# Optimization experiments

Hardware: AMD Instinct MI355X
Metric: run time of the kernel (lower is better)

Reference implementation:

```python
import jax, jax.numpy as jnp
import numpy as np

B, C, L = 256, 256, 512
EPS = 1e-5

def setup_inputs() -> dict:
    key = jax.random.key(0)
    k1, k2, k3, k4 = jax.random.split(key, 4)
    x = jax.random.normal(k1, (B, C, L), dtype=jnp.float32)
    idx = jax.random.randint(k2, (B, L), 0, L + 1, dtype=jnp.int32)  # L == pad slot
    # Conv1d(2C, C, 1): weight [C, 2C], bias [C]
    W = jax.random.normal(k3, (C, 2 * C), dtype=jnp.float32) * (1.0 / np.sqrt(2 * C))
    b = jax.random.normal(k4, (C,), dtype=jnp.float32) * 0.01
    return {"x": x, "idx": idx, "W": W, "b": b}

def reference(x, idx, W, b):
    # collect_neighbours: pad length dim with one zero column, gather per (b, l)
    x_pad = jnp.pad(x, ((0, 0), (0, 0), (0, 1)))            # [B, C, L+1]
    nbr = jnp.take_along_axis(x_pad, idx[:, None, :].astype(jnp.int32), axis=2)  # [B, C, L]
    cat = jnp.concatenate([x, nbr], axis=1)                 # [B, 2C, L]
    # 1x1 Conv1d == channel matmul
    y = jnp.einsum('oc,bcl->bol', W, cat) + b[None, :, None]  # [B, C, L]
    # InstanceNorm1d (affine=False): normalize over L per (b, c), biased var
    mu = jnp.mean(y, axis=2, keepdims=True)
    var = jnp.mean(jnp.square(y - mu), axis=2, keepdims=True)
    y = (y - mu) * jax.lax.rsqrt(var + EPS)
    return jax.nn.relu(y)
```

## Files before the change

### kernel.cpp

```cpp
#include <hip/hip_runtime.h>
#include <hip/hip_bf16.h>
#include <stdint.h>

typedef __bf16 bf16x8 __attribute__((ext_vector_type(8)));
typedef float  f32x4  __attribute__((ext_vector_type(4)));

__device__ __forceinline__ uint32_t cvt2(float a, float b) {
    __hip_bfloat162 h = __float22bfloat162_rn(make_float2(a, b));
    uint32_t u; __builtin_memcpy(&u, &h, 4); return u;
}
__device__ __forceinline__ float bflo(uint32_t u) { uint32_t t = u << 16;         float f; __builtin_memcpy(&f, &t, 4); return f; }
__device__ __forceinline__ float bfhi(uint32_t u) { uint32_t t = u & 0xffff0000u; float f; __builtin_memcpy(&f, &t, 4); return f; }
__device__ __forceinline__ int swz(int u) { return u ^ ((u >> 3) & 7); }

__device__ __forceinline__ void gload_lds16(const void* g, void* l) {
    __builtin_amdgcn_global_load_lds(
        (const __attribute__((address_space(1))) uint32_t*)g,
        (__attribute__((address_space(3))) uint32_t*)l,
        16, 0, 0);
}

__global__ __launch_bounds__(256, 4)
void pack_transpose(const float* __restrict__ x, const float* __restrict__ W,
                    unsigned short* __restrict__ xT, unsigned short* __restrict__ wT)
{
    const int tid = threadIdx.x;
    const int id  = blockIdx.x;
    if (id < 2048) {
        const int b  = ((id >> 6) << 3) + (id & 7);
        const int kc = (id >> 3) & 7;
        const int s2 = tid >> 6, l4 = tid & 63;
        const float* src0 = x + ((size_t)b << 17) + ((size_t)((kc << 5) + (s2 << 3)) << 9);
        unsigned short* dst0 = xT + (((size_t)(b << 5) + (kc << 2) + s2) << 12);
        f32x4 xr[16];
        #pragma unroll
        for (int lh = 0; lh < 2; ++lh) {
            const int l0 = (lh << 8) + (l4 << 2);
            #pragma unroll
            for (int j = 0; j < 8; ++j)
                xr[(lh << 3) + j] = __builtin_nontemporal_load((const f32x4*)(src0 + (j << 9) + l0));
        }
        #pragma unroll
        for (int lh = 0; lh < 2; ++lh) {
            const int l0 = (lh << 8) + (l4 << 2);
            #pragma unroll
            for (int lv = 0; lv < 4; ++lv) {
                uint4 p;
                p.x = cvt2(xr[(lh << 3) + 0][lv], xr[(lh << 3) + 1][lv]);
                p.y = cvt2(xr[(lh << 3) + 2][lv], xr[(lh << 3) + 3][lv]);
                p.z = cvt2(xr[(lh << 3) + 4][lv], xr[(lh << 3) + 5][lv]);
                p.w = cvt2(xr[(lh << 3) + 6][lv], xr[(lh << 3) + 7][lv]);
                *(uint4*)(dst0 + ((l0 + lv) << 3)) = p;
            }
        }
    } else {
        const int og = id - 2048;
        const int r = tid & 63, sg = tid >> 6;
        const float* wrow = W + ((size_t)((og << 5) + (r & 31)) << 9) + ((r >> 5) << 8);
        #pragma unroll
        for (int ss = 0; ss < 8; ++ss) {
            const int s = (sg << 3) + ss;
            float4 f0 = *(const float4*)(wrow + (s << 3));
            float4 f1 = *(const float4*)(wrow + (s << 3) + 4);
            uint4 p;
            p.x = cvt2(f0.x, f0.y); p.y = cvt2(f0.z, f0.w);
            p.z = cvt2(f1.x, f1.y); p.w = cvt2(f1.z, f1.w);
            *(uint4*)(wT + (((((og << 5) + s) << 6) + r) << 3)) = p;
        }
    }
}

__global__ __launch_bounds__(256, 2)
void edge_gemm(const unsigned short* __restrict__ xT,
               const unsigned short* __restrict__ wT,
               const int* __restrict__ idx,
               float* __restrict__ out)
{
    __shared__ __align__(16) unsigned char smem[76032];
    unsigned short* y2 = (unsigned short*)(smem + 36864);
    float* red         = (float*)(smem + 75776);

    const int tid  = threadIdx.x;
    const int wv   = tid >> 6;
    const int lane = tid & 63;
    const int m    = lane & 15;
    const int q    = lane >> 4;

    const int id  = blockIdx.x;
    const int rem = id & 63;
    const int b   = ((id >> 6) << 3) + (rem & 7);
    const int og  = rem >> 3;
    const int o0  = og << 5;

    const char* xb = (const char*)xT + ((size_t)b << 18);
    const char* wb = (const char*)wT + (og << 15);

    const int offS = (wv << 10) + (lane << 4);

    int iv[8];
    #pragma unroll
    for (int nt = 0; nt < 8; ++nt)
        iv[nt] = idx[((size_t)b << 9) + (wv << 7) + (nt << 4) + m];

    f32x4 acc[4][8];
    #pragma unroll
    for (int mt = 0; mt < 4; ++mt)
        #pragma unroll
        for (int nt = 0; nt < 8; ++nt)
            acc[mt][nt] = (f32x4){0.f, 0.f, 0.f, 0.f};

    auto stage = [&](int c, int bsel) {
        char* Bl = (char*)smem + bsel * 36864;
        const char* Bg = xb + ((size_t)c << 15);
        #pragma unroll
        for (int i = 0; i < 8; ++i)
            gload_lds16(Bg + (i << 12) + offS, Bl + (i << 12) + offS);
        gload_lds16(wb + (c << 12) + offS, Bl + 32768 + offS);
    };

    stage(0, 1);
    stage(1, 0);

    #pragma unroll
    for (int kc = 0; kc < 8; ++kc) {
        const int bsel = (kc + 1) & 1;
        if (kc < 7) asm volatile("s_waitcnt vmcnt(9)" ::: "memory");
        else        asm volatile("s_waitcnt vmcnt(0)" ::: "memory");
        __builtin_amdgcn_s_barrier();
        __builtin_amdgcn_sched_barrier(0);

        const unsigned short* B0 = (const unsigned short*)((const char*)smem + bsel * 36864);
        const unsigned short* A0 = B0 + 16384;
        bf16x8 av[4], bv[8];
        #pragma unroll
        for (int mt = 0; mt < 4; ++mt)
            av[mt] = *(const bf16x8*)(A0 + (q << 9) + (((mt << 4) + m) << 3));
        #pragma unroll
        for (int nt = 0; nt < 8; ++nt)
            bv[nt] = *(const bf16x8*)(B0 + (q << 12) + (((wv << 7) + (nt << 4) + m) << 3));
        #pragma unroll
        for (int mt = 0; mt < 4; ++mt)
            #pragma unroll
            for (int nt = 0; nt < 8; ++nt)
                acc[mt][nt] = __builtin_amdgcn_mfma_f32_16x16x32_bf16(av[mt], bv[nt], acc[mt][nt], 0, 0, 0);

        __builtin_amdgcn_sched_barrier(0);
        if (kc < 7) {
            asm volatile("s_waitcnt lgkmcnt(0)" ::: "memory");
            __builtin_amdgcn_s_barrier();
            if (kc < 6) stage(kc + 2, bsel);
        }
    }

    #pragma unroll
    for (int mt = 2; mt < 4; ++mt)
        #pragma unroll
        for (int nt = 0; nt < 8; ++nt) {
            int col  = (wv << 7) + (nt << 4) + m;
            int row0 = ((mt - 2) << 4) + (q << 2);
            uint2 p;
            p.x = cvt2(acc[mt][nt][0], acc[mt][nt][1]);
            p.y = cvt2(acc[mt][nt][2], acc[mt][nt][3]);
            *(uint2*)(y2 + col * 38 + row0) = p;
        }
    __syncthreads();

    float vvl[2][8][4];
    float s_[2][4], q_[2][4];
    #pragma unroll
    for (int mt = 0; mt < 2; ++mt)
        #pragma unroll
        for (int r4 = 0; r4 < 4; ++r4) { s_[mt][r4] = 0.f; q_[mt][r4] = 0.f; }

    #pragma unroll
    for (int nt = 0; nt < 8; ++nt) {
        int  c   = iv[nt];
        bool inb = (c < 512);
        int  cc  = inb ? c : 0;
        #pragma unroll
        for (int mt = 0; mt < 2; ++mt) {
            uint2 g = *(const uint2*)(y2 + cc * 38 + (mt << 4) + (q << 2));
            float gv[4];
            gv[0] = inb ? bflo(g.x) : 0.f;
            gv[1] = inb ? bfhi(g.x) : 0.f;
            gv[2] = inb ? bflo(g.y) : 0.f;
            gv[3] = inb ? bfhi(g.y) : 0.f;
            #pragma unroll
            for (int r4 = 0; r4 < 4; ++r4) {
                float val = acc[mt][nt][r4] + gv[r4];
                vvl[mt][nt][r4] = val;
                s_[mt][r4] += val;
                q_[mt][r4] += val * val;
            }
        }
    }

    #pragma unroll
    for (int mt = 0; mt < 2; ++mt)
        #pragma unroll
        for (int r4 = 0; r4 < 4; ++r4) {
            float s = s_[mt][r4], ss = q_[mt][r4];
            #pragma unroll
            for (int off = 1; off < 16; off <<= 1) {
                s  += __shfl_xor(s,  off, 64);
                ss += __shfl_xor(ss, off, 64);
            }
            if (m == 0) {
                int r = (mt << 4) + (q << 2) + r4;
                red[(r << 3) + (wv << 1)]     = s;
                red[(r << 3) + (wv << 1) + 1] = ss;
            }
        }
    __syncthreads();

    #pragma unroll
    for (int mt = 0; mt < 2; ++mt)
        #pragma unroll
        for (int r4 = 0; r4 < 4; ++r4) {
            int r = (mt << 4) + (q << 2) + r4;
            float S = red[(r << 3)]     + red[(r << 3) + 2] + red[(r << 3) + 4] + red[(r << 3) + 6];
            float Q = red[(r << 3) + 1] + red[(r << 3) + 3] + red[(r << 3) + 5] + red[(r << 3) + 7];
            float mu  = S * (1.0f / 512.0f);
            float var = Q * (1.0f / 512.0f) - mu * mu;
            float rs  = rsqrtf(var + 1e-5f);
            float* op = out + (((size_t)(b << 8) + o0 + r) << 9) + (wv << 7) + m;
            #pragma unroll
            for (int nt = 0; nt < 8; ++nt) {
                float t = (vvl[mt][nt][r4] - mu) * rs;
                __builtin_nontemporal_store(fmaxf(t, 0.0f), op + (nt << 4));
            }
        }
}

__global__ __launch_bounds__(256, 2)
void edgeconv_fused(const float* __restrict__ x,
                    const int*   __restrict__ idx,
                    const float* __restrict__ W,
                    float*       __restrict__ out)
{
    __shared__ __align__(16) unsigned char smem[65536];
    unsigned short* wlds = (unsigned short*)smem;
    unsigned short* xTl  = (unsigned short*)(smem + 32768);
    unsigned short* y2   = (unsigned short*)smem;
    float*          red  = (float*)(smem + 38912);

    const int tid  = threadIdx.x;
    const int wv   = tid >> 6;
    const int lane = tid & 63;
    const int m    = lane & 15;
    const int q    = lane >> 4;

    const int id  = blockIdx.x;
    const int rem = id & 63;
    const int b   = ((id >> 6) << 3) + (rem & 7);
    const int o0  = (rem >> 3) << 5;

    const float* xb = x + ((size_t)b << 17);

    #pragma unroll
    for (int i = 0; i < 16; ++i) {
        int r = (i << 2) + wv;
        const float4 f = *(const float4*)(W + ((size_t)(o0 + (r & 31)) << 9)
                                            + ((r >> 5) << 8) + (lane << 2));
        uint2 p; p.x = cvt2(f.x, f.y); p.y = cvt2(f.z, f.w);
        int sl = lane >> 1;
        *(uint2*)(wlds + (sl << 9) + ((swz(r) ^ (sl & 7)) << 3) + ((lane & 1) << 2)) = p;
    }

    f32x4 acc[4][8];
    #pragma unroll
    for (int mt = 0; mt < 4; ++mt)
        #pragma unroll
        for (int nt = 0; nt < 8; ++nt)
            acc[mt][nt] = (f32x4){0.f, 0.f, 0.f, 0.f};

    float4 xr0[8], xr1[8];
    auto loadg = [&](int kc, int g, float4* xr) {
        int gid = (g << 8) + tid;
        int s2  = gid >> 7;
        int l4  = gid & 127;
        const float* base = xb + ((size_t)((kc << 5) + (s2 << 3)) << 9) + (l4 << 2);
        #pragma unroll
        for (int j = 0; j < 8; ++j) xr[j] = *(const float4*)(base + (j << 9));
    };
    auto storeg = [&](int g, const float4* xr) {
        int gid = (g << 8) + tid;
        int s2  = gid >> 7;
        int l4  = gid & 127;
        #pragma unroll
        for (int lv = 0; lv < 4; ++lv) {
            int l = (l4 << 2) + lv;
            uint4 p;
            p.x = cvt2((&xr[0].x)[lv], (&xr[1].x)[lv]);
            p.y = cvt2((&xr[2].x)[lv], (&xr[3].x)[lv]);
            p.z = cvt2((&xr[4].x)[lv], (&xr[5].x)[lv]);
            p.w = cvt2((&xr[6].x)[lv], (&xr[7].x)[lv]);
            *(uint4*)(xTl + (s2 << 12) + (swz(l) << 3)) = p;
        }
    };

    loadg(0, 0, xr0);
    loadg(0, 1, xr1);
    storeg(0, xr0);
    storeg(1, xr1);
    __syncthreads();

    for (int kc = 0; kc < 8; ++kc) {
        if (kc < 7) loadg(kc + 1, 0, xr0);

        bf16x8 av[4], bv[8];
        #pragma unroll
        for (int mt = 0; mt < 4; ++mt) {
            int sl = (kc << 2) + q;
            av[mt] = *(const bf16x8*)(wlds + (sl << 9) + ((swz((mt << 4) + m) ^ (sl & 7)) << 3));
        }
        #pragma unroll
        for (int nt = 0; nt < 8; ++nt)
            bv[nt] = *(const bf16x8*)(xTl + (q << 12) + (swz((wv << 7) + (nt << 4) + m) << 3));

        #pragma unroll
        for (int mt = 0; mt < 4; ++mt)
            #pragma unroll
            for (int nt = 0; nt < 8; ++nt)
                acc[mt][nt] = __builtin_amdgcn_mfma_f32_16x16x32_bf16(av[mt], bv[nt], acc[mt][nt], 0, 0, 0);

        if (kc < 7) loadg(kc + 1, 1, xr1);
        __syncthreads();
        if (kc < 7) {
            storeg(0, xr0);
            storeg(1, xr1);
            __syncthreads();
        }
    }

    int iv[8];
    #pragma unroll
    for (int nt = 0; nt < 8; ++nt)
        iv[nt] = idx[((size_t)b << 9) + (wv << 7) + (nt << 4) + m];

    #pragma unroll
    for (int mt = 2; mt < 4; ++mt)
        #pragma unroll
        for (int nt = 0; nt < 8; ++nt) {
            int col  = (wv << 7) + (nt << 4) + m;
            int row0 = ((mt - 2) << 4) + (q << 2);
            uint2 p;
            p.x = cvt2(acc[mt][nt][0], acc[mt][nt][1]);
            p.y = cvt2(acc[mt][nt][2], acc[mt][nt][3]);
            *(uint2*)(y2 + col * 36 + row0) = p;
        }
    __syncthreads();

    float vvl[2][8][4];
    float s_[2][4], q_[2][4];
    #pragma unroll
    for (int mt = 0; mt < 2; ++mt)
        #pragma unroll
        for (int r4 = 0; r4 < 4; ++r4) { s_[mt][r4] = 0.f; q_[mt][r4] = 0.f; }

    #pragma unroll
    for (int nt = 0; nt < 8; ++nt) {
        int  c   = iv[nt];
        bool inb = (c < 512);
        int  cc  = inb ? c : 0;
        #pragma unroll
        for (int mt = 0; mt < 2; ++mt) {
            uint2 g = *(const uint2*)(y2 + cc * 36 + (mt << 4) + (q << 2));
            float gv[4];
            gv[0] = inb ? bflo(g.x) : 0.f;
            gv[1] = inb ? bfhi(g.x) : 0.f;
            gv[2] = inb ? bflo(g.y) : 0.f;
            gv[3] = inb ? bfhi(g.y) : 0.f;
            #pragma unroll
            for (int r4 = 0; r4 < 4; ++r4) {
                float val = acc[mt][nt][r4] + gv[r4];
                vvl[mt][nt][r4] = val;
                s_[mt][r4] += val;
                q_[mt][r4] += val * val;
            }
        }
    }

    #pragma unroll
    for (int mt = 0; mt < 2; ++mt)
        #pragma unroll
        for (int r4 = 0; r4 < 4; ++r4) {
            float s = s_[mt][r4], ss = q_[mt][r4];
            #pragma unroll
            for (int off = 1; off < 16; off <<= 1) {
                s  += __shfl_xor(s,  off, 64);
                ss += __shfl_xor(ss, off, 64);
            }
            if (m == 0) {
                int r = (mt << 4) + (q << 2) + r4;
                red[(r << 3) + (wv << 1)]     = s;
                red[(r << 3) + (wv << 1) + 1] = ss;
            }
        }
    __syncthreads();

    #pragma unroll
    for (int mt = 0; mt < 2; ++mt)
        #pragma unroll
        for (int r4 = 0; r4 < 4; ++r4) {
            int r = (mt << 4) + (q << 2) + r4;
            float S = red[(r << 3)]     + red[(r << 3) + 2] + red[(r << 3) + 4] + red[(r << 3) + 6];
            float Q = red[(r << 3) + 1] + red[(r << 3) + 3] + red[(r << 3) + 5] + red[(r << 3) + 7];
            float mu  = S * (1.0f / 512.0f);
            float var = Q * (1.0f / 512.0f) - mu * mu;
            float rs  = rsqrtf(var + 1e-5f);
            float* op = out + (((size_t)(b << 8) + o0 + r) << 9) + (wv << 7) + m;
            #pragma unroll
            for (int nt = 0; nt < 8; ++nt) {
                float t = (vvl[mt][nt][r4] - mu) * rs;
                op[nt << 4] = fmaxf(t, 0.0f);
            }
        }
}

extern "C" void kernel_launch(void* const* d_in, const int* in_sizes, int n_in,
                              void* d_out, int out_size, void* d_ws, size_t ws_size,
                              hipStream_t stream) {
    const float* x   = (const float*)d_in[0];
    const int*   idx = (const int*)  d_in[1];
    const float* W   = (const float*)d_in[2];
    float* out = (float*)d_out;

    const size_t xT_bytes = (size_t)256 * 32 * 512 * 8 * 2;
    const size_t wT_bytes = (size_t)8 * 32 * 64 * 8 * 2;

    if (ws_size >= xT_bytes + wT_bytes) {
        unsigned short* xT = (unsigned short*)d_ws;
        unsigned short* wT = (unsigned short*)((char*)d_ws + xT_bytes);
        pack_transpose<<<dim3(2056), dim3(256), 0, stream>>>(x, W, xT, wT);
        edge_gemm<<<dim3(2048), dim3(256), 0, stream>>>(xT, wT, idx, out);
    } else {
        edgeconv_fused<<<dim3(2048), dim3(256), 0, stream>>>(x, idx, W, out);
    }
}
```

Baseline: 305.6 us.

## Share staged x tile across two output groups in 512-thread GEMM blocks

Edge GEMM blocks grow to 512 threads, with two 4-wave groups computing adjacent 32-row output slices against one shared staged x tile. This halves global reads of the activation tile and the number of blocks. The hand-tuned vmcnt/s_barrier pipeline is replaced by a plain double-buffered loop synchronised with __syncthreads, and the non-temporal output stores become ordinary stores. The launch bound of (512,4) may force a very tight register budget with 128 accumulator floats per thread, so spilling is a risk.

```diff
diff --git a/kernel.cpp b/kernel.cpp
--- a/kernel.cpp
+++ b/kernel.cpp
@@ -70,37 +70,39 @@
     }
 }
 
-__global__ __launch_bounds__(256, 2)
+__global__ __launch_bounds__(512, 4)
 void edge_gemm(const unsigned short* __restrict__ xT,
                const unsigned short* __restrict__ wT,
                const int* __restrict__ idx,
                float* __restrict__ out)
 {
-    __shared__ __align__(16) unsigned char smem[76032];
-    unsigned short* y2 = (unsigned short*)(smem + 36864);
-    float* red         = (float*)(smem + 75776);
+    __shared__ __align__(16) unsigned char smem[81920];
 
     const int tid  = threadIdx.x;
     const int wv   = tid >> 6;
     const int lane = tid & 63;
     const int m    = lane & 15;
     const int q    = lane >> 4;
+    const int g    = wv >> 2;
+    const int wsub = wv & 3;
 
     const int id  = blockIdx.x;
-    const int rem = id & 63;
-    const int b   = ((id >> 6) << 3) + (rem & 7);
-    const int og  = rem >> 3;
+    const int rem = id & 31;
+    const int b   = ((id >> 5) << 3) + (rem & 7);
+    const int ogp = rem >> 3;
+    const int og  = (ogp << 1) + g;
     const int o0  = og << 5;
 
     const char* xb = (const char*)xT + ((size_t)b << 18);
-    const char* wb = (const char*)wT + (og << 15);
-
-    const int offS = (wv << 10) + (lane << 4);
+    const char* wp = (const char*)wT + ((size_t)og << 15);
+
+    unsigned short* y2  = (unsigned short*)(smem + g * 40960);
+    float*          red = (float*)(smem + g * 40960 + 38912);
 
     int iv[8];
     #pragma unroll
     for (int nt = 0; nt < 8; ++nt)
-        iv[nt] = idx[((size_t)b << 9) + (wv << 7) + (nt << 4) + m];
+        iv[nt] = idx[((size_t)b << 9) + (wsub << 7) + (nt << 4) + m];
 
     f32x4 acc[4][8];
     #pragma unroll
@@ -109,54 +111,51 @@
         for (int nt = 0; nt < 8; ++nt)
             acc[mt][nt] = (f32x4){0.f, 0.f, 0.f, 0.f};
 
+    const int offB = tid << 4;
+    const int offA = (g << 12) + (wsub << 10) + (lane << 4);
+
     auto stage = [&](int c, int bsel) {
-        char* Bl = (char*)smem + bsel * 36864;
+        char* base = (char*)smem + bsel * 40960;
         const char* Bg = xb + ((size_t)c << 15);
         #pragma unroll
-        for (int i = 0; i < 8; ++i)
-            gload_lds16(Bg + (i << 12) + offS, Bl + (i << 12) + offS);
-        gload_lds16(wb + (c << 12) + offS, Bl + 32768 + offS);
+        for (int i = 0; i < 4; ++i)
+            gload_lds16(Bg + (i << 13) + offB, base + (i << 13) + offB);
+        gload_lds16(wp + (c << 12) + (wsub << 10) + (lane << 4), base + 32768 + offA);
     };
 
     stage(0, 1);
-    stage(1, 0);
+    __syncthreads();
 
     #pragma unroll
     for (int kc = 0; kc < 8; ++kc) {
         const int bsel = (kc + 1) & 1;
-        if (kc < 7) asm volatile("s_waitcnt vmcnt(9)" ::: "memory");
-        else        asm volatile("s_waitcnt vmcnt(0)" ::: "memory");
-        __builtin_amdgcn_s_barrier();
-        __builtin_amdgcn_sched_barrier(0);
-
-        const unsigned short* B0 = (const unsigned short*)((const char*)smem + bsel * 36864);
+        if (kc < 7) stage(kc + 1, bsel ^ 1);
+
+        const unsigned short* B0 = (const unsigned short*)((const char*)smem + bsel * 40960);
         const unsigned short* A0 = B0 + 16384;
         bf16x8 av[4], bv[8];
         #pragma unroll
         for (int mt = 0; mt < 4; ++mt)
-            av[mt] = *(const bf16x8*)(A0 + (q << 9) + (((mt << 4) + m) << 3));
+            av[mt] = *(const bf16x8*)(A0 + (g << 11) + (q << 9) + (((mt << 4) + m) << 3));
         #pragma unroll
         for (int nt = 0; nt < 8; ++nt)
-            bv[nt] = *(const bf16x8*)(B0 + (q << 12) + (((wv << 7) + (nt << 4) + m) << 3));
+            bv[nt] = *(const bf16x8*)(B0 + (q << 12) + (((wsub << 7) + (nt << 4) + m) << 3));
         #pragma unroll
         for (int mt = 0; mt < 4; ++mt)
             #pragma unroll
             for (int nt = 0; nt < 8; ++nt)
                 acc[mt][nt] = __builtin_amdgcn_mfma_f32_16x16x32_bf16(av[mt], bv[nt], acc[mt][nt], 0, 0, 0);
 
-        __builtin_amdgcn_sched_barrier(0);
-        if (kc < 7) {
-            asm volatile("s_waitcnt lgkmcnt(0)" ::: "memory");
-            __builtin_amdgcn_s_barrier();
-            if (kc < 6) stage(kc + 2, bsel);
-        }
-    }
+        if (kc < 7) __syncthreads();
+    }
+
+    __syncthreads();
 
     #pragma unroll
     for (int mt = 2; mt < 4; ++mt)
         #pragma unroll
         for (int nt = 0; nt < 8; ++nt) {
-            int col  = (wv << 7) + (nt << 4) + m;
+            int col  = (wsub << 7) + (nt << 4) + m;
             int row0 = ((mt - 2) << 4) + (q << 2);
             uint2 p;
             p.x = cvt2(acc[mt][nt][0], acc[mt][nt][1]);
@@ -179,12 +178,12 @@
         int  cc  = inb ? c : 0;
         #pragma unroll
         for (int mt = 0; mt < 2; ++mt) {
-            uint2 g = *(const uint2*)(y2 + cc * 38 + (mt << 4) + (q << 2));
+            uint2 gg = *(const uint2*)(y2 + cc * 38 + (mt << 4) + (q << 2));
             float gv[4];
-            gv[0] = inb ? bflo(g.x) : 0.f;
-            gv[1] = inb ? bfhi(g.x) : 0.f;
-            gv[2] = inb ? bflo(g.y) : 0.f;
-            gv[3] = inb ? bfhi(g.y) : 0.f;
+            gv[0] = inb ? bflo(gg.x) : 0.f;
+            gv[1] = inb ? bfhi(gg.x) : 0.f;
+            gv[2] = inb ? bflo(gg.y) : 0.f;
+            gv[3] = inb ? bfhi(gg.y) : 0.f;
             #pragma unroll
             for (int r4 = 0; r4 < 4; ++r4) {
                 float val = acc[mt][nt][r4] + gv[r4];
@@ -207,8 +206,8 @@
             }
             if (m == 0) {
                 int r = (mt << 4) + (q << 2) + r4;
-                red[(r << 3) + (wv << 1)]     = s;
-                red[(r << 3) + (wv << 1) + 1] = ss;
+                red[(r << 3) + (wsub << 1)]     = s;
+                red[(r << 3) + (wsub << 1) + 1] = ss;
             }
         }
     __syncthreads();
@@ -223,11 +222,11 @@
             float mu  = S * (1.0f / 512.0f);
             float var = Q * (1.0f / 512.0f) - mu * mu;
             float rs  = rsqrtf(var + 1e-5f);
-            float* op = out + (((size_t)(b << 8) + o0 + r) << 9) + (wv << 7) + m;
+            float* op = out + (((size_t)(b << 8) + o0 + r) << 9) + (wsub << 7) + m;
             #pragma unroll
             for (int nt = 0; nt < 8; ++nt) {
                 float t = (vvl[mt][nt][r4] - mu) * rs;
-                __builtin_nontemporal_store(fmaxf(t, 0.0f), op + (nt << 4));
+                op[nt << 4] = fmaxf(t, 0.0f);
             }
         }
 }
@@ -433,7 +432,7 @@
         unsigned short* xT = (unsigned short*)d_ws;
         unsigned short* wT = (unsigned short*)((char*)d_ws + xT_bytes);
         pack_transpose<<<dim3(2056), dim3(256), 0, stream>>>(x, W, xT, wT);
-        edge_gemm<<<dim3(2048), dim3(256), 0, stream>>>(xT, wT, idx, out);
+        edge_gemm<<<dim3(1024), dim3(512), 0, stream>>>(xT, wT, idx, out);
     } else {
         edgeconv_fused<<<dim3(2048), dim3(256), 0, stream>>>(x, idx, W, out);
     }
```

Result: slower. 497.3 us (+62.7%).

## Split edge_gemm across 8 waves with fewer accumulators and simpler double buffering

Applied to the files above, without the earlier changes.

The GEMM kernel now uses 512 threads per block. Each of the 8 waves owns 64 columns, so each wave holds half as many accumulators and the per-thread register pressure drops, which is meant to allow more resident waves. The hand-tuned vmcnt-based two-stage prefetch is replaced by a single-ahead prefetch with plain __syncthreads, and the stored vvl values are dropped: the gathered neighbour term is recomputed from LDS in a second pass. The y2 buffer now reuses the staging buffer's LDS space. The trade-offs are less overlap between memory loads and compute, extra LDS reads, and regular stores in place of nontemporal ones.

```diff
diff --git a/kernel.cpp b/kernel.cpp
--- a/kernel.cpp
+++ b/kernel.cpp
@@ -70,15 +70,15 @@
     }
 }
 
-__global__ __launch_bounds__(256, 2)
+__global__ __launch_bounds__(512, 4)
 void edge_gemm(const unsigned short* __restrict__ xT,
                const unsigned short* __restrict__ wT,
                const int* __restrict__ idx,
                float* __restrict__ out)
 {
-    __shared__ __align__(16) unsigned char smem[76032];
-    unsigned short* y2 = (unsigned short*)(smem + 36864);
-    float* red         = (float*)(smem + 75776);
+    __shared__ __align__(16) unsigned char smem[73728];
+    unsigned short* y2  = (unsigned short*)smem;
+    float*          red = (float*)(smem + 40960);
 
     const int tid  = threadIdx.x;
     const int wv   = tid >> 6;
@@ -95,68 +95,62 @@
     const char* xb = (const char*)xT + ((size_t)b << 18);
     const char* wb = (const char*)wT + (og << 15);
 
-    const int offS = (wv << 10) + (lane << 4);
-
-    int iv[8];
-    #pragma unroll
-    for (int nt = 0; nt < 8; ++nt)
-        iv[nt] = idx[((size_t)b << 9) + (wv << 7) + (nt << 4) + m];
-
-    f32x4 acc[4][8];
+    int iv[4];
+    #pragma unroll
+    for (int nt = 0; nt < 4; ++nt)
+        iv[nt] = idx[((size_t)b << 9) + (wv << 6) + (nt << 4) + m];
+
+    f32x4 acc[4][4];
     #pragma unroll
     for (int mt = 0; mt < 4; ++mt)
         #pragma unroll
-        for (int nt = 0; nt < 8; ++nt)
+        for (int nt = 0; nt < 4; ++nt)
             acc[mt][nt] = (f32x4){0.f, 0.f, 0.f, 0.f};
 
+    const int offB = tid << 4;
     auto stage = [&](int c, int bsel) {
-        char* Bl = (char*)smem + bsel * 36864;
+        char* base = (char*)smem + bsel * 36864;
         const char* Bg = xb + ((size_t)c << 15);
         #pragma unroll
-        for (int i = 0; i < 8; ++i)
-            gload_lds16(Bg + (i << 12) + offS, Bl + (i << 12) + offS);
-        gload_lds16(wb + (c << 12) + offS, Bl + 32768 + offS);
+        for (int i = 0; i < 4; ++i)
+            gload_lds16(Bg + (i << 13) + offB, base + (i << 13) + offB);
+        if (tid < 256)
+            gload_lds16(wb + (c << 12) + offB, base + 32768 + offB);
     };
 
-    stage(0, 1);
-    stage(1, 0);
+    stage(0, 0);
+    __syncthreads();
 
     #pragma unroll
     for (int kc = 0; kc < 8; ++kc) {
-        const int bsel = (kc + 1) & 1;
-        if (kc < 7) asm volatile("s_waitcnt vmcnt(9)" ::: "memory");
-        else        asm volatile("s_waitcnt vmcnt(0)" ::: "memory");
-        __builtin_amdgcn_s_barrier();
-        __builtin_amdgcn_sched_barrier(0);
+        const int bsel = kc & 1;
+        if (kc < 7) stage(kc + 1, bsel ^ 1);
 
         const unsigned short* B0 = (const unsigned short*)((const char*)smem + bsel * 36864);
         const unsigned short* A0 = B0 + 16384;
-        bf16x8 av[4], bv[8];
+        bf16x8 av[4], bv[4];
         #pragma unroll
         for (int mt = 0; mt < 4; ++mt)
             av[mt] = *(const bf16x8*)(A0 + (q << 9) + (((mt << 4) + m) << 3));
         #pragma unroll
-        for (int nt = 0; nt < 8; ++nt)
-            bv[nt] = *(const bf16x8*)(B0 + (q << 12) + (((wv << 7) + (nt << 4) + m) << 3));
+        for (int nt = 0; nt < 4; ++nt)
+            bv[nt] = *(const bf16x8*)(B0 + (q << 12) + (((wv << 6) + (nt << 4) + m) << 3));
         #pragma unroll
         for (int mt = 0; mt < 4; ++mt)
             #pragma unroll
-            for (int nt = 0; nt < 8; ++nt)
+            for (int nt = 0; nt < 4; ++nt)
                 acc[mt][nt] = __builtin_amdgcn_mfma_f32_16x16x32_bf16(av[mt], bv[nt], acc[mt][nt], 0, 0, 0);
 
-        __builtin_amdgcn_sched_barrier(0);
-        if (kc < 7) {
-            asm volatile("s_waitcnt lgkmcnt(0)" ::: "memory");
-            __builtin_amdgcn_s_barrier();
-            if (kc < 6) stage(kc + 2, bsel);
-        }
-    }
+        if (kc < 7) __syncthreads();
+    }
+
+    __syncthreads();
 
     #pragma unroll
     for (int mt = 2; mt < 4; ++mt)
         #pragma unroll
-        for (int nt = 0; nt < 8; ++nt) {
-            int col  = (wv << 7) + (nt << 4) + m;
+        for (int nt = 0; nt < 4; ++nt) {
+            int col  = (wv << 6) + (nt << 4) + m;
             int row0 = ((mt - 2) << 4) + (q << 2);
             uint2 p;
             p.x = cvt2(acc[mt][nt][0], acc[mt][nt][1]);
@@ -165,7 +159,6 @@
         }
     __syncthreads();
 
-    float vvl[2][8][4];
     float s_[2][4], q_[2][4];
     #pragma unroll
     for (int mt = 0; mt < 2; ++mt)
@@ -173,7 +166,7 @@
         for (int r4 = 0; r4 < 4; ++r4) { s_[mt][r4] = 0.f; q_[mt][r4] = 0.f; }
 
     #pragma unroll
-    for (int nt = 0; nt < 8; ++nt) {
+    for (int nt = 0; nt < 4; ++nt) {
         int  c   = iv[nt];
         bool inb = (c < 512);
         int  cc  = inb ? c : 0;
@@ -188,7 +181,6 @@
             #pragma unroll
             for (int r4 = 0; r4 < 4; ++r4) {
                 float val = acc[mt][nt][r4] + gv[r4];
-                vvl[mt][nt][r4] = val;
                 s_[mt][r4] += val;
                 q_[mt][r4] += val * val;
             }
@@ -207,27 +199,49 @@
             }
             if (m == 0) {
                 int r = (mt << 4) + (q << 2) + r4;
-                red[(r << 3) + (wv << 1)]     = s;
-                red[(r << 3) + (wv << 1) + 1] = ss;
-            }
-        }
-    __syncthreads();
-
+                red[(r << 4) + (wv << 1)]     = s;
+                red[(r << 4) + (wv << 1) + 1] = ss;
+            }
+        }
+    __syncthreads();
+
+    float mu[2][4], rs[2][4];
     #pragma unroll
     for (int mt = 0; mt < 2; ++mt)
         #pragma unroll
         for (int r4 = 0; r4 < 4; ++r4) {
             int r = (mt << 4) + (q << 2) + r4;
-            float S = red[(r << 3)]     + red[(r << 3) + 2] + red[(r << 3) + 4] + red[(r << 3) + 6];
-            float Q = red[(r << 3) + 1] + red[(r << 3) + 3] + red[(r << 3) + 5] + red[(r << 3) + 7];
-            float mu  = S * (1.0f / 512.0f);
-            float var = Q * (1.0f / 512.0f) - mu * mu;
-            float rs  = rsqrtf(var + 1e-5f);
-            float* op = out + (((size_t)(b << 8) + o0 + r) << 9) + (wv << 7) + m;
-            #pragma unroll
-            for (int nt = 0; nt < 8; ++nt) {
-                float t = (vvl[mt][nt][r4] - mu) * rs;
-                __builtin_nontemporal_store(fmaxf(t, 0.0f), op + (nt << 4));
+            float S = 0.f, Q = 0.f;
+            #pragma unroll
+            for (int w = 0; w < 8; ++w) {
+                S += red[(r << 4) + (w << 1)];
+                Q += red[(r << 4) + (w << 1) + 1];
+            }
+            float muv = S * (1.0f / 512.0f);
+            float var = Q * (1.0f / 512.0f) - muv * muv;
+            mu[mt][r4] = muv;
+            rs[mt][r4] = rsqrtf(var + 1e-5f);
+        }
+
+    #pragma unroll
+    for (int mt = 0; mt < 2; ++mt)
+        #pragma unroll
+        for (int nt = 0; nt < 4; ++nt) {
+            int  c   = iv[nt];
+            bool inb = (c < 512);
+            int  cc  = inb ? c : 0;
+            uint2 g = *(const uint2*)(y2 + cc * 38 + (mt << 4) + (q << 2));
+            float gv[4];
+            gv[0] = inb ? bflo(g.x) : 0.f;
+            gv[1] = inb ? bfhi(g.x) : 0.f;
+            gv[2] = inb ? bflo(g.y) : 0.f;
+            gv[3] = inb ? bfhi(g.y) : 0.f;
+            #pragma unroll
+            for (int r4 = 0; r4 < 4; ++r4) {
+                int r = (mt << 4) + (q << 2) + r4;
+                float val = acc[mt][nt][r4] + gv[r4];
+                float t   = (val - mu[mt][r4]) * rs[mt][r4];
+                out[(((size_t)(b << 8) + o0 + r) << 9) + (wv << 6) + (nt << 4) + m] = fmaxf(t, 0.0f);
             }
         }
 }
@@ -433,7 +447,7 @@
         unsigned short* xT = (unsigned short*)d_ws;
         unsigned short* wT = (unsigned short*)((char*)d_ws + xT_bytes);
         pack_transpose<<<dim3(2056), dim3(256), 0, stream>>>(x, W, xT, wT);
-        edge_gemm<<<dim3(2048), dim3(256), 0, stream>>>(xT, wT, idx, out);
+        edge_gemm<<<dim3(2048), dim3(512), 0, stream>>>(xT, wT, idx, out);
     } else {
         edgeconv_fused<<<dim3(2048), dim3(256), 0, stream>>>(x, idx, W, out);
     }
```

Result: slower. 327.7 us (+7.2%).
